# Kernel tuning notes

Hardware: AMD Instinct MI355X
Metric: run time of the kernel (lower is better)

The kernel has to match this reference:

```python
import jax, jax.numpy as jnp
import numpy as np

TAU = 2.0
V_TH = 0.5
BN_EPS = 1e-5
ALPHA = 2.0  # spikingjelly surrogate.ATan default

@jax.custom_vjp
def spike_fn(x):
    # Heaviside forward, ATan surrogate backward (defined for fwdbwd parity)
    return (x >= 0.0).astype(x.dtype)

def _spike_fwd(x):
    return spike_fn(x), x

def _spike_bwd(x, g):
    return (g * (ALPHA / 2.0) / (1.0 + (jnp.pi / 2.0 * ALPHA * x) ** 2),)

spike_fn.defvjp(_spike_fwd, _spike_bwd)

def lif_multistep(x_seq):
    # MultiStepLIFNode: v <- v + (x - v)/tau ; spike = H(v - v_th) ; hard reset v<-v*(1-sg(spike))
    def step(v, x_t):
        v = v + (x_t - v) / TAU
        s = spike_fn(v - V_TH)
        v = v * (1.0 - jax.lax.stop_gradient(s))  # detach_reset=True, v_reset=0
        return v, s
    v0 = jnp.zeros_like(x_seq[0])
    _, spikes = jax.lax.scan(step, v0, x_seq)
    return spikes

def setup_inputs() -> dict:
    key = jax.random.key(0)
    k1, k2, k3 = jax.random.split(key, 3)
    T, B, N, D = 4, 64, 256, 512
    x = jax.random.normal(k1, (T, B, N, D), jnp.float32)
    mx = jax.random.normal(k2, (N, B, T, D), jnp.float32)
    W = jax.random.normal(k3, (D, D), jnp.float32) / np.sqrt(D).astype(np.float32)
    gamma = jnp.ones((D,), jnp.float32)
    beta = jnp.zeros((D,), jnp.float32)
    return {"x": x, "mx": mx, "W": W, "gamma": gamma, "beta": beta}

def reference(x, mx, W, gamma, beta):
    # mx: [N,B,T,D] -> transpose(0,2) -> [T,B,N,D]
    mxt = jnp.transpose(mx, (2, 1, 0, 3))
    # Linear (no bias): [T,B,N,D] @ W^T
    h = jnp.einsum('tbnd,ed->tbne', mxt, W)
    # BatchNorm1d(D) in training mode: stats over (T*B, N) per channel D (biased var)
    mean = h.mean(axis=(0, 1, 2))
    var = h.var(axis=(0, 1, 2))
    hn = (h - mean) * jax.lax.rsqrt(var + BN_EPS) * gamma + beta
    # LIF recurrence over T
    s = lif_multistep(hn)  # [T,B,N,D] binary spikes
    return x * s
```

## Files before the change

kernel.cpp:

```cpp
#include <hip/hip_runtime.h>
#include <math.h>

namespace {
constexpr int TDIM = 4, BDIM = 64, NDIM = 256, DDIM = 512;
constexpr int MROWS = 65536;
constexpr long long BND = 8388608LL;
constexpr double BN_EPS = 1e-5;

constexpr int BM = 64, BNT = 128, BK = 32;
constexpr int APITCH = BK + 2;
constexpr int WPITCH = BNT + 4;
constexpr int LDS_BYTES = (BM * APITCH + BK * WPITCH) * 8;

constexpr int BM3 = 128, BN3 = 64, BK3 = 16;
constexpr int AP3 = BM3 + 1;
constexpr int WP3 = BN3 + 1;

constexpr int NSA = 6, NSW = 5;
constexpr long long APL = 33554432LL;
constexpr long long WPL = 262144LL;
constexpr int CH8 = 22528;
}

typedef double d4 __attribute__((ext_vector_type(4)));
typedef int i32x4 __attribute__((ext_vector_type(4)));
typedef int i32x16 __attribute__((ext_vector_type(16)));

#define GLOAD16(g, d) __builtin_amdgcn_global_load_lds( \
    (const __attribute__((address_space(1))) void*)(g), \
    (__attribute__((address_space(3))) void*)(d), 16, 0, 0)

__global__ void probe_k(double* __restrict__ rowmap)
{
    const int l = threadIdx.x;
    d4 z = {0.0, 0.0, 0.0, 0.0};
    d4 dr = __builtin_amdgcn_mfma_f64_16x16x4f64((double)(l & 15), 1.0, z, 0, 0, 0);
#pragma unroll
    for (int r = 0; r < 4; ++r)
        rowmap[l * 4 + r] = dr[r] * 0.25;
}

__global__ void probe8_k(double* __restrict__ irow8, double* __restrict__ icol8)
{
    const int l = threadIdx.x;
    i32x16 z;
#pragma unroll
    for (int r = 0; r < 16; ++r) z[r] = 0;
    const int mb = (l & 31) * 0x01010101;
    const int ob = 0x01010101;
    i32x4 am = {mb, mb, mb, mb};
    i32x4 a1 = {ob, ob, ob, ob};
    i32x16 d1 = __builtin_amdgcn_mfma_i32_32x32x32_i8(am, a1, z, 0, 0, 0);
#pragma unroll
    for (int r = 0; r < 16; ++r)
        irow8[l * 16 + r] = (double)d1[r] / 32.0;
    i32x16 d2 = __builtin_amdgcn_mfma_i32_32x32x32_i8(a1, am, z, 0, 0, 0);
    icol8[l] = (double)d2[0] / 32.0;
}

__global__ __launch_bounds__(256)
void slice_a_k(const float* __restrict__ src, char* __restrict__ dst)
{
    const int ri  = threadIdx.x & 63;
    const int ks0 = threadIdx.x >> 6;
    const long long row = (long long)blockIdx.x * 64 + ri;
#pragma unroll 1
    for (int it = 0; it < 8; ++it) {
        const int kseg = it * 4 + ks0;
        const float* sp = src + row * DDIM + kseg * 16;
        union { char c[16]; i32x4 v; } pk[NSA];
#pragma unroll
        for (int e = 0; e < 16; ++e) {
            double V = (double)sp[e] * 4.0;
            double u = rint(V);
            double r = V - u;
            pk[0].c[e] = (char)(int)u;
#pragma unroll
            for (int s = 1; s < NSA; ++s) {
                r *= 128.0;
                u = rint(r);
                r -= u;
                pk[s].c[e] = (char)(int)u;
            }
        }
        const long long base = (long long)blockIdx.x * 32768 + kseg * 1024 + ri * 16;
#pragma unroll
        for (int s = 0; s < NSA; ++s)
            *(i32x4*)(dst + (long long)s * APL + base) = pk[s].v;
    }
}

__global__ __launch_bounds__(256)
void slice_w_k(const float* __restrict__ src, char* __restrict__ dst)
{
    const int cbk  = blockIdx.x >> 3;
    const int kgrp = blockIdx.x & 7;
    const int ci   = threadIdx.x & 63;
    const int kseg = kgrp * 4 + (threadIdx.x >> 6);
    const float* sp = src + (long long)(cbk * 64 + ci) * DDIM + kseg * 16;
    union { char c[16]; i32x4 v; } pk[NSW];
#pragma unroll
    for (int e = 0; e < 16; ++e) {
        double V = (double)sp[e] * 256.0;
        double u = rint(V);
        double r = V - u;
        pk[0].c[e] = (char)(int)u;
#pragma unroll
        for (int s = 1; s < NSW; ++s) {
            r *= 128.0;
            u = rint(r);
            r -= u;
            pk[s].c[e] = (char)(int)u;
        }
    }
    const long long base = (long long)cbk * 32768 + kseg * 1024 + ci * 16;
#pragma unroll
    for (int s = 0; s < NSW; ++s)
        *(i32x4*)(dst + (long long)s * WPL + base) = pk[s].v;
}

__device__ __forceinline__ void stage8(const char* Asl, const char* Wsl,
                                       char* buf, long long aTile, long long wTile,
                                       int c, int w, int l)
{
    char* bufA = buf;
    char* bufW = buf + NSA * 2048;
    for (int idx = w; idx < 22; idx += 4) {
        if (idx < 12) {
            const int s = idx >> 1, j = idx & 1;
            const char* g = Asl + (long long)s * APL + aTile
                          + (long long)(2 * c + j) * 1024 + l * 16;
            GLOAD16(g, bufA + s * 2048 + j * 1024);
        } else {
            const int e = idx - 12, t = e >> 1, j = e & 1;
            const char* g = Wsl + (long long)t * WPL + wTile
                          + (long long)(2 * c + j) * 1024 + l * 16;
            GLOAD16(g, bufW + t * 2048 + j * 1024);
        }
    }
}

__global__ __launch_bounds__(256, 3)
void gemm8_k(const char* __restrict__ Asl, const char* __restrict__ Wsl,
             double* __restrict__ hbuf, double* __restrict__ sums,
             const double* __restrict__ irow8, const double* __restrict__ icol8)
{
    __shared__ __align__(16) char sm[2][CH8];

    const int tid = threadIdx.x;
    const int bid = blockIdx.x;
    const int rb  = ((bid >> 6) << 3) | (bid & 7);
    const int cb  = (bid >> 3) & 7;

    const int w  = tid >> 6;
    const int l  = tid & 63;
    const int wr = w >> 1;
    const int wc = w & 1;

    const long long aTile = (long long)rb * 32768;
    const long long wTile = (long long)cb * 32768;

    i32x16 acc[6];
#pragma unroll
    for (int g = 0; g < 6; ++g)
#pragma unroll
        for (int r = 0; r < 16; ++r) acc[g][r] = 0;

    const int roA = (l >> 5) * 1024 + (32 * wr + (l & 31)) * 16;
    const int roW = (l >> 5) * 1024 + (32 * wc + (l & 31)) * 16;

    stage8(Asl, Wsl, sm[0], aTile, wTile, 0, w, l);
    __syncthreads();

    for (int c = 0; c < 16; ++c) {
        if (c < 15)
            stage8(Asl, Wsl, sm[(c + 1) & 1], aTile, wTile, c + 1, w, l);

        const char* bA = sm[c & 1];
        const char* bW = sm[c & 1] + NSA * 2048;
        i32x4 af[NSA], wf[NSW];
#pragma unroll
        for (int s = 0; s < NSA; ++s)
            af[s] = *(const i32x4*)(bA + s * 2048 + roA);
#pragma unroll
        for (int t = 0; t < NSW; ++t)
            wf[t] = *(const i32x4*)(bW + t * 2048 + roW);
#pragma unroll
        for (int s = 0; s < NSA; ++s)
#pragma unroll
            for (int t = 0; t < NSW; ++t)
                if (s + t <= 5)
                    acc[s + t] = __builtin_amdgcn_mfma_i32_32x32x32_i8(
                                     af[s], wf[t], acc[s + t], 0, 0, 0);
        __syncthreads();
    }

    int irw[16];
#pragma unroll
    for (int r = 0; r < 16; ++r) irw[r] = (int)irow8[l * 16 + r];
    const int icl = (int)icol8[l];

    const double C7 = 1.0 / 128.0, CMB = 1.0 / 1024.0;
    double lsum = 0.0, lsq = 0.0;
    const int colg = cb * 64 + 32 * wc + icl;
    const int row0 = rb * 64 + 32 * wr;
#pragma unroll
    for (int r = 0; r < 16; ++r) {
        double t = (double)acc[5][r];
        t = fma(t, C7, (double)acc[4][r]);
        t = fma(t, C7, (double)acc[3][r]);
        t = fma(t, C7, (double)acc[2][r]);
        t = fma(t, C7, (double)acc[1][r]);
        t = fma(t, C7, (double)acc[0][r]);
        const double h = t * CMB;
        hbuf[(size_t)(row0 + irw[r]) * DDIM + colg] = h;
        lsum += h;
        lsq = fma(h, h, lsq);
    }

    __syncthreads();
    double* Ss = (double*)sm;
    const int ctr = wr * 2 + (l >> 5);
    const int cloc = 32 * wc + icl;
    Ss[cloc * 4 + ctr] = lsum;
    Ss[256 + cloc * 4 + ctr] = lsq;
    __syncthreads();
    if (tid < 64) {
        double s = 0.0, q = 0.0;
#pragma unroll
        for (int k = 0; k < 4; ++k) {
            s += Ss[tid * 4 + k];
            q += Ss[256 + tid * 4 + k];
        }
        atomicAdd(&sums[cb * 64 + tid], s);
        atomicAdd(&sums[512 + cb * 64 + tid], q);
    }
}

__global__ __launch_bounds__(256, 2)
void gemm3_k(const float* __restrict__ mx, const float* __restrict__ Wm,
             double* __restrict__ hbuf, double* __restrict__ sums,
             const double* __restrict__ rowmap)
{
    __shared__ double Atr[BK3 * AP3];
    __shared__ double Wt [BK3 * WP3];

    const int tid = threadIdx.x;
    const int bid = blockIdx.x;
    const int rb  = ((bid >> 6) << 3) | (bid & 7);
    const int cb  = (bid >> 3) & 7;
    const int row0 = rb * BM3;
    const int col0 = cb * BN3;

    const int w  = tid >> 6;
    const int l  = tid & 63;
    const int wr = w >> 1;
    const int wc = w & 1;
    const int lr = l & 15;
    const int kq = l >> 4;

    int irow[4];
#pragma unroll
    for (int r = 0; r < 4; ++r)
        irow[r] = (int)rowmap[l * 4 + r];

    const int arow = tid >> 1;
    const int af   = (tid & 1) * 8;
    const int wrow = tid >> 2;
    const int wf   = (tid & 3) * 4;
    const float* aSrc = mx + (size_t)(row0 + arow) * DDIM + af;
    const float* wSrc = Wm + (size_t)(col0 + wrow) * DDIM + wf;

    d4 acc[4][2];
#pragma unroll
    for (int i = 0; i < 4; ++i)
#pragma unroll
        for (int j = 0; j < 2; ++j) acc[i][j] = (d4){0.0, 0.0, 0.0, 0.0};

    float4 pa0 = *(const float4*)(aSrc + 0);
    float4 pa1 = *(const float4*)(aSrc + 4);
    float4 pw  = *(const float4*)(wSrc + 0);

    for (int kk = 0; kk < DDIM; kk += BK3) {
        __syncthreads();
        Atr[(af + 0) * AP3 + arow] = (double)pa0.x;
        Atr[(af + 1) * AP3 + arow] = (double)pa0.y;
        Atr[(af + 2) * AP3 + arow] = (double)pa0.z;
        Atr[(af + 3) * AP3 + arow] = (double)pa0.w;
        Atr[(af + 4) * AP3 + arow] = (double)pa1.x;
        Atr[(af + 5) * AP3 + arow] = (double)pa1.y;
        Atr[(af + 6) * AP3 + arow] = (double)pa1.z;
        Atr[(af + 7) * AP3 + arow] = (double)pa1.w;
        Wt[(wf + 0) * WP3 + wrow] = (double)pw.x;
        Wt[(wf + 1) * WP3 + wrow] = (double)pw.y;
        Wt[(wf + 2) * WP3 + wrow] = (double)pw.z;
        Wt[(wf + 3) * WP3 + wrow] = (double)pw.w;
        __syncthreads();

        if (kk + BK3 < DDIM) {
            pa0 = *(const float4*)(aSrc + kk + BK3 + 0);
            pa1 = *(const float4*)(aSrc + kk + BK3 + 4);
            pw  = *(const float4*)(wSrc + kk + BK3 + 0);
        }

#pragma unroll
        for (int ks = 0; ks < BK3 / 4; ++ks) {
            const int kabs = ks * 4 + kq;
            double a[4], b[2];
#pragma unroll
            for (int i = 0; i < 4; ++i)
                a[i] = Atr[kabs * AP3 + 64 * wr + 16 * i + lr];
#pragma unroll
            for (int j = 0; j < 2; ++j)
                b[j] = Wt[kabs * WP3 + 32 * wc + 16 * j + lr];
#pragma unroll
            for (int i = 0; i < 4; ++i)
#pragma unroll
                for (int j = 0; j < 2; ++j)
                    acc[i][j] = __builtin_amdgcn_mfma_f64_16x16x4f64(
                                    a[i], b[j], acc[i][j], 0, 0, 0);
        }
    }

#pragma unroll
    for (int i = 0; i < 4; ++i) {
#pragma unroll
        for (int j = 0; j < 2; ++j) {
            const size_t cbase = (size_t)col0 + 32 * wc + 16 * j + lr;
            const size_t rbase = (size_t)row0 + 64 * wr + 16 * i;
#pragma unroll
            for (int r = 0; r < 4; ++r)
                hbuf[(rbase + irow[r]) * DDIM + cbase] = acc[i][j][r];
        }
    }

    __syncthreads();
    double* Ssum = Atr;
    double* Ssq  = Atr + 512;
    const int ctr = wr * 4 + kq;
#pragma unroll
    for (int j = 0; j < 2; ++j) {
        const int cloc = 32 * wc + 16 * j + lr;
        double s = 0.0, q = 0.0;
#pragma unroll
        for (int i = 0; i < 4; ++i)
#pragma unroll
            for (int r = 0; r < 4; ++r) {
                const double v = acc[i][j][r];
                s += v;
                q = fma(v, v, q);
            }
        Ssum[cloc * 8 + ctr] = s;
        Ssq [cloc * 8 + ctr] = q;
    }
    __syncthreads();
    if (tid < 64) {
        double s = 0.0, q = 0.0;
#pragma unroll
        for (int c = 0; c < 8; ++c) {
            s += Ssum[tid * 8 + c];
            q += Ssq [tid * 8 + c];
        }
        atomicAdd(&sums[col0 + tid], s);
        atomicAdd(&sums[512 + col0 + tid], q);
    }
}

template<int MODE>
__global__ __launch_bounds__(256)
void gemm_k(const float* __restrict__ mx, const float* __restrict__ Wm,
            double* __restrict__ hbuf, double* __restrict__ sums,
            const double* __restrict__ scale, const double* __restrict__ shiftv,
            const float* __restrict__ x, float* __restrict__ out)
{
    __shared__ __align__(16) char smem[LDS_BYTES];
    double (*Ald)[APITCH] = reinterpret_cast<double(*)[APITCH]>(smem);
    double (*Wld)[WPITCH] = reinterpret_cast<double(*)[WPITCH]>(smem + (size_t)BM * APITCH * 8);

    const int tid  = threadIdx.x;
    const int rb   = blockIdx.x >> 2;
    const int cb   = blockIdx.x & 3;
    const int row0 = rb * BM;
    const int col0 = cb * BNT;

    const int arow = tid >> 2;
    const int ak   = (tid & 3) * 8;
    const int erow = tid >> 1;
    const int wk   = (tid & 1) * 16;

    const float* aSrc = mx + (size_t)(row0 + arow) * DDIM;
    const float* wSrc = Wm + (size_t)(col0 + erow) * DDIM;

    const int rg = tid >> 4;
    const int cg = tid & 15;

    double acc[4][8];
#pragma unroll
    for (int i = 0; i < 4; ++i)
#pragma unroll
        for (int j = 0; j < 8; ++j) acc[i][j] = 0.0;

    for (int kk = 0; kk < DDIM; kk += BK) {
        const float4 a0 = *(const float4*)(aSrc + kk + ak);
        const float4 a1 = *(const float4*)(aSrc + kk + ak + 4);
        const float4 w0 = *(const float4*)(wSrc + kk + wk);
        const float4 w1 = *(const float4*)(wSrc + kk + wk + 4);
        const float4 w2 = *(const float4*)(wSrc + kk + wk + 8);
        const float4 w3 = *(const float4*)(wSrc + kk + wk + 12);
        __syncthreads();
        Ald[arow][ak + 0] = (double)a0.x; Ald[arow][ak + 1] = (double)a0.y;
        Ald[arow][ak + 2] = (double)a0.z; Ald[arow][ak + 3] = (double)a0.w;
        Ald[arow][ak + 4] = (double)a1.x; Ald[arow][ak + 5] = (double)a1.y;
        Ald[arow][ak + 6] = (double)a1.z; Ald[arow][ak + 7] = (double)a1.w;
        const float wfv[16] = {w0.x, w0.y, w0.z, w0.w, w1.x, w1.y, w1.z, w1.w,
                               w2.x, w2.y, w2.z, w2.w, w3.x, w3.y, w3.z, w3.w};
#pragma unroll
        for (int q = 0; q < 16; ++q) Wld[wk + q][erow] = (double)wfv[q];
        __syncthreads();

#pragma unroll 4
        for (int d = 0; d < BK; ++d) {
            double a[4], wv[8];
#pragma unroll
            for (int i = 0; i < 4; ++i) a[i] = Ald[rg * 4 + i][d];
#pragma unroll
            for (int j = 0; j < 8; ++j) wv[j] = Wld[d][cg * 8 + j];
#pragma unroll
            for (int i = 0; i < 4; ++i)
#pragma unroll
                for (int j = 0; j < 8; ++j)
                    acc[i][j] = fma(a[i], wv[j], acc[i][j]);
        }
    }

    if (MODE <= 1) {
        __syncthreads();
        double* scr = reinterpret_cast<double*>(smem);
#pragma unroll
        for (int j = 0; j < 8; ++j) {
            const double s = acc[0][j] + acc[1][j] + acc[2][j] + acc[3][j];
            const double q = acc[0][j]*acc[0][j] + acc[1][j]*acc[1][j]
                           + acc[2][j]*acc[2][j] + acc[3][j]*acc[3][j];
            scr[(cg * 8 + j) * 16 + rg] = s;
            scr[2048 + (cg * 8 + j) * 16 + rg] = q;
        }
        __syncthreads();
        if (tid < 128) {
            double s = 0.0, q = 0.0;
#pragma unroll
            for (int r = 0; r < 16; ++r) {
                s += scr[tid * 16 + r];
                q += scr[2048 + tid * 16 + r];
            }
            atomicAdd(&sums[col0 + tid], s);
            atomicAdd(&sums[512 + col0 + tid], q);
        }
    }

    if (MODE == 2) {
        const int p  = rb * 16 + rg;
        const int nn = p >> 6;
        const int bb = p & 63;
#pragma unroll
        for (int j = 0; j < 8; ++j) {
            const int e = col0 + cg * 8 + j;
            const double sc = scale[e];
            const double sh = shiftv[e];
            const size_t basex = (size_t)bb * (NDIM * DDIM) + (size_t)nn * DDIM + e;
            double v = 0.0;
#pragma unroll
            for (int t = 0; t < 4; ++t) {
                const double hn = fma(acc[t][j], sc, sh);
                v = v + (hn - v) / 2.0;
                const bool s = (v - 0.5) >= 0.0;
                const size_t xi = (size_t)t * BND + basex;
                out[xi] = s ? x[xi] : 0.0f;
                if (s) v = 0.0;
            }
        }
    }
}

__global__ void zero_k(double* sums)
{
    const int i = blockIdx.x * 256 + threadIdx.x;
    if (i < 1024) sums[i] = 0.0;
}

__global__ void stat_k(const double* __restrict__ sums,
                       const float* __restrict__ gamma, const float* __restrict__ beta,
                       double* __restrict__ scale, double* __restrict__ shiftv)
{
    const int e = blockIdx.x * 256 + threadIdx.x;
    if (e < 512) {
        const double mean = sums[e] * (1.0 / 65536.0);
        const double msq  = sums[512 + e] * (1.0 / 65536.0);
        const double var  = msq - mean * mean;
        const double inv  = 1.0 / sqrt(var + BN_EPS);
        const double g    = (double)gamma[e] * inv;
        scale[e]  = g;
        shiftv[e] = (double)beta[e] - mean * g;
    }
}

__global__ __launch_bounds__(256)
void lifh_k(const double* __restrict__ hbuf, const double* __restrict__ scale,
            const double* __restrict__ shiftv, const float* __restrict__ x,
            float* __restrict__ out)
{
    const size_t i = (size_t)blockIdx.x * 256 + threadIdx.x;
    const int e  = (int)(i & 511);
    const size_t p = i >> 9;
    const int nn = (int)(p >> 6);
    const int bb = (int)(p & 63);
    const double sc = scale[e];
    const double sh = shiftv[e];
    const double* hp = hbuf + p * 2048 + e;
    const size_t basex = (size_t)bb * (NDIM * DDIM) + (size_t)nn * DDIM + e;
    double v = 0.0;
#pragma unroll
    for (int t = 0; t < 4; ++t) {
        const double hn = fma(hp[(size_t)t * 512], sc, sh);
        v = v + (hn - v) / 2.0;
        const bool s = (v - 0.5) >= 0.0;
        const size_t xi = (size_t)t * BND + basex;
        out[xi] = s ? x[xi] : 0.0f;
        if (s) v = 0.0;
    }
}

extern "C" void kernel_launch(void* const* d_in, const int* in_sizes, int n_in,
                              void* d_out, int out_size, void* d_ws, size_t ws_size,
                              hipStream_t stream)
{
    const float* x     = (const float*)d_in[0];
    const float* mx    = (const float*)d_in[1];
    const float* Wm    = (const float*)d_in[2];
    const float* gamma = (const float*)d_in[3];
    const float* beta  = (const float*)d_in[4];
    float* out = (float*)d_out;

    char* ws = (char*)d_ws;
    double* sums   = (double*)ws;
    double* scale  = (double*)(ws + 8192);
    double* shiftv = scale + 512;
    double* rowmap = (double*)(ws + 16384);
    double* irow8  = (double*)(ws + 18432);
    double* icol8  = (double*)(ws + 26624);
    double* hbuf   = (double*)(ws + 32768);

    const size_t HBSZ   = (size_t)MROWS * DDIM * 8;
    const size_t OFF_AS = 32768 + HBSZ;
    const size_t ASSZ   = (size_t)NSA * APL;
    const size_t OFF_WS = OFF_AS + ASSZ;
    const size_t WSSZ   = (size_t)NSW * WPL;
    const size_t need8  = OFF_WS + WSSZ;
    const size_t need_h = 32768 + HBSZ;

    hipLaunchKernelGGL(zero_k, dim3(4), dim3(256), 0, stream, sums);

    if (ws_size >= need8) {
        char* Asl = ws + OFF_AS;
        char* Wsl = ws + OFF_WS;
        hipLaunchKernelGGL(probe8_k, dim3(1), dim3(64), 0, stream, irow8, icol8);
        hipLaunchKernelGGL(slice_a_k, dim3(1024), dim3(256), 0, stream, mx, Asl);
        hipLaunchKernelGGL(slice_w_k, dim3(64), dim3(256), 0, stream, Wm, Wsl);
        hipLaunchKernelGGL(gemm8_k, dim3(8192), dim3(256), 0, stream,
                           Asl, Wsl, hbuf, sums, irow8, icol8);
        hipLaunchKernelGGL(stat_k, dim3(2), dim3(256), 0, stream,
                           sums, gamma, beta, scale, shiftv);
        hipLaunchKernelGGL(lifh_k, dim3(32768), dim3(256), 0, stream,
                           hbuf, scale, shiftv, x, out);
    } else if (ws_size >= need_h) {
        hipLaunchKernelGGL(probe_k, dim3(1), dim3(64), 0, stream, rowmap);
        hipLaunchKernelGGL(gemm3_k, dim3(4096), dim3(256), 0, stream,
                           mx, Wm, hbuf, sums, rowmap);
        hipLaunchKernelGGL(stat_k, dim3(2), dim3(256), 0, stream,
                           sums, gamma, beta, scale, shiftv);
        hipLaunchKernelGGL(lifh_k, dim3(32768), dim3(256), 0, stream,
                           hbuf, scale, shiftv, x, out);
    } else {
        hipLaunchKernelGGL((gemm_k<0>), dim3(4096), dim3(256), 0, stream,
                           mx, Wm, nullptr, sums, nullptr, nullptr, nullptr, nullptr);
        hipLaunchKernelGGL(stat_k, dim3(2), dim3(256), 0, stream,
                           sums, gamma, beta, scale, shiftv);
        hipLaunchKernelGGL((gemm_k<2>), dim3(4096), dim3(256), 0, stream,
                           mx, Wm, nullptr, nullptr, scale, shiftv, x, out);
    }
}
```

Before: 514.6 us.

## Restructure int8 GEMM staging with precomputed pointers and vmcnt-based double buffering

Replaces the per-iteration stage8 loop with a templated Stager that precomputes global and LDS offsets and advances pointers by a fixed stride. The chunk loads are redistributed so waves 0-1 issue 6 and waves 2-3 issue 5. The main loop now keeps two chunks in flight, prefetching into the buffer just consumed. It uses explicit s_waitcnt vmcnt counts and raw s_barrier in place of __syncthreads, which waited on all outstanding loads. The aim is deeper overlap of global-to-LDS loads with MFMA work and less address arithmetic, at the cost of hand-tuned waitcnt correctness and wave-divergent code paths.

```diff
diff --git a/kernel.cpp b/kernel.cpp
--- a/kernel.cpp
+++ b/kernel.cpp
@@ -119,24 +119,74 @@
         *(i32x4*)(dst + (long long)s * WPL + base) = pk[s].v;
 }
 
-__device__ __forceinline__ void stage8(const char* Asl, const char* Wsl,
-                                       char* buf, long long aTile, long long wTile,
-                                       int c, int w, int l)
-{
-    char* bufA = buf;
-    char* bufW = buf + NSA * 2048;
-    for (int idx = w; idx < 22; idx += 4) {
-        if (idx < 12) {
-            const int s = idx >> 1, j = idx & 1;
-            const char* g = Asl + (long long)s * APL + aTile
-                          + (long long)(2 * c + j) * 1024 + l * 16;
-            GLOAD16(g, bufA + s * 2048 + j * 1024);
+template<int NW>
+struct Stager {
+    const char* gp[NW];
+    int lo[NW];
+    __device__ __forceinline__ void init(int w0, const char* Asl, const char* Wsl,
+                                         long long aT, long long wT, int l)
+    {
+#pragma unroll
+        for (int i = 0; i < NW; ++i) {
+            const int idx = w0 + i;
+            if (idx < 12) {
+                gp[i] = Asl + (long long)(idx >> 1) * APL + aT
+                      + (long long)(idx & 1) * 1024 + l * 16;
+                lo[i] = (idx >> 1) * 2048 + (idx & 1) * 1024;
+            } else {
+                const int e = idx - 12;
+                gp[i] = Wsl + (long long)(e >> 1) * WPL + wT
+                      + (long long)(e & 1) * 1024 + l * 16;
+                lo[i] = 12288 + (e >> 1) * 2048 + (e & 1) * 1024;
+            }
+        }
+    }
+    __device__ __forceinline__ void issue(char* buf)
+    {
+#pragma unroll
+        for (int i = 0; i < NW; ++i) {
+            GLOAD16(gp[i], buf + lo[i]);
+            gp[i] += 2048;
+        }
+    }
+};
+
+template<int NW>
+__device__ __forceinline__ void gemm8_loop(Stager<NW>& st, char* smb,
+                                           i32x16 (&acc)[6], int roA, int roW)
+{
+#pragma unroll 2
+    for (int c = 0; c < 16; ++c) {
+        const char* bA = smb + (c & 1) * CH8;
+        const char* bW = bA + 12288;
+        i32x4 af[NSA], wf[NSW];
+#pragma unroll
+        for (int s = 0; s < NSA; ++s)
+            af[s] = *(const i32x4*)(bA + s * 2048 + roA);
+#pragma unroll
+        for (int t = 0; t < NSW; ++t)
+            wf[t] = *(const i32x4*)(bW + t * 2048 + roW);
+#pragma unroll
+        for (int s = 0; s < NSA; ++s)
+#pragma unroll
+            for (int t = 0; t < NSW; ++t)
+                if (s + t <= 5)
+                    acc[s + t] = __builtin_amdgcn_mfma_i32_32x32x32_i8(
+                                     af[s], wf[t], acc[s + t], 0, 0, 0);
+        if (c == 15) break;
+        asm volatile("s_barrier" ::: "memory");
+        if (c < 14) {
+            st.issue(smb + (c & 1) * CH8);
+            if constexpr (NW == 6)
+                asm volatile("s_waitcnt vmcnt(6)" ::: "memory");
+            else
+                asm volatile("s_waitcnt vmcnt(5)" ::: "memory");
         } else {
-            const int e = idx - 12, t = e >> 1, j = e & 1;
-            const char* g = Wsl + (long long)t * WPL + wTile
-                          + (long long)(2 * c + j) * 1024 + l * 16;
-            GLOAD16(g, bufW + t * 2048 + j * 1024);
-        }
+            asm volatile("s_waitcnt vmcnt(0)" ::: "memory");
+        }
+        __builtin_amdgcn_sched_barrier(0);
+        asm volatile("s_barrier" ::: "memory");
+        __builtin_amdgcn_sched_barrier(0);
     }
 }
 
@@ -169,30 +219,27 @@
     const int roA = (l >> 5) * 1024 + (32 * wr + (l & 31)) * 16;
     const int roW = (l >> 5) * 1024 + (32 * wc + (l & 31)) * 16;
 
-    stage8(Asl, Wsl, sm[0], aTile, wTile, 0, w, l);
-    __syncthreads();
-
-    for (int c = 0; c < 16; ++c) {
-        if (c < 15)
-            stage8(Asl, Wsl, sm[(c + 1) & 1], aTile, wTile, c + 1, w, l);
-
-        const char* bA = sm[c & 1];
-        const char* bW = sm[c & 1] + NSA * 2048;
-        i32x4 af[NSA], wf[NSW];
-#pragma unroll
-        for (int s = 0; s < NSA; ++s)
-            af[s] = *(const i32x4*)(bA + s * 2048 + roA);
-#pragma unroll
-        for (int t = 0; t < NSW; ++t)
-            wf[t] = *(const i32x4*)(bW + t * 2048 + roW);
-#pragma unroll
-        for (int s = 0; s < NSA; ++s)
-#pragma unroll
-            for (int t = 0; t < NSW; ++t)
-                if (s + t <= 5)
-                    acc[s + t] = __builtin_amdgcn_mfma_i32_32x32x32_i8(
-                                     af[s], wf[t], acc[s + t], 0, 0, 0);
-        __syncthreads();
+    char* smb = &sm[0][0];
+    if (w < 2) {
+        Stager<6> st;
+        st.init(6 * w, Asl, Wsl, aTile, wTile, l);
+        st.issue(smb);
+        st.issue(smb + CH8);
+        asm volatile("s_waitcnt vmcnt(6)" ::: "memory");
+        __builtin_amdgcn_sched_barrier(0);
+        asm volatile("s_barrier" ::: "memory");
+        __builtin_amdgcn_sched_barrier(0);
+        gemm8_loop<6>(st, smb, acc, roA, roW);
+    } else {
+        Stager<5> st;
+        st.init(12 + 5 * (w - 2), Asl, Wsl, aTile, wTile, l);
+        st.issue(smb);
+        st.issue(smb + CH8);
+        asm volatile("s_waitcnt vmcnt(5)" ::: "memory");
+        __builtin_amdgcn_sched_barrier(0);
+        asm volatile("s_barrier" ::: "memory");
+        __builtin_amdgcn_sched_barrier(0);
+        gemm8_loop<5>(st, smb, acc, roA, roW);
     }
 
     int irw[16];
```

Result: faster. 480.0 us (-6.7%).
